# Optimization experiments

Hardware: AMD Instinct MI355X
Metric: run time of the kernel (lower is better)

The kernel has to match this reference:

```python
import jax, jax.numpy as jnp
import numpy as np

D, H, O, E, K = 1024, 4096, 1024, 12, 4
N = 8192


def setup_inputs() -> dict:
    key = jax.random.key(0)
    ks = jax.random.split(key, 7)
    s = 0.02
    return {
        "x": jax.random.normal(ks[0], (N, D), dtype=jnp.float32),
        "gate_w": jax.random.normal(ks[1], (D, E), dtype=jnp.float32) * s,
        "gate_b": jnp.zeros((E,), dtype=jnp.float32),
        "w1": jax.random.normal(ks[2], (E, D, H), dtype=jnp.float32) * s,
        "b1": jnp.zeros((E, H), dtype=jnp.float32),
        "w2": jax.random.normal(ks[3], (E, H, O), dtype=jnp.float32) * s,
        "b2": jnp.zeros((E, O), dtype=jnp.float32),
    }


def reference(x, gate_w, gate_b, w1, b1, w2, b2):
    # Gating: full softmax over all experts, then mask to top-k and renormalize
    scores = x @ gate_w + gate_b                      # [N, E]
    _, topk_idx = jax.lax.top_k(scores, K)            # [N, K]
    mask = jnp.sum(jax.nn.one_hot(topk_idx, E, dtype=scores.dtype), axis=-2)  # [N, E]
    weights = jax.nn.softmax(scores, axis=-1) * mask
    weights = weights / (jnp.sum(weights, axis=-1, keepdims=True) + 1e-8)

    # Dense all-expert MLP (faithful to original: every expert on every token)
    h = jax.nn.relu(jnp.einsum("nd,edh->neh", x, w1) + b1)  # [N, E, H]
    outs = jnp.einsum("neh,eho->neo", h, w2) + b2           # [N, E, O]

    return jnp.einsum("ne,neo->no", weights, outs)          # [N, O]
```

## Files before the change

kernel.cpp:

```cpp
#include <hip/hip_runtime.h>
#include <stdint.h>

#define D_DIM 1024
#define H_DIM 4096
#define O_DIM 1024
#define E_NUM 12
#define TOPK 4
#define N_TOK 8192

#define PAIR_CAP 34304

typedef __bf16 bf16x8 __attribute__((ext_vector_type(8)));
typedef float f32x4 __attribute__((ext_vector_type(4)));
typedef unsigned short u16x8 __attribute__((ext_vector_type(8)));

typedef __attribute__((address_space(3))) unsigned int lds_uint;
typedef __attribute__((address_space(1))) const unsigned int glob_uint;

static __device__ __forceinline__ unsigned short f2b(float f) {
  union { float f; unsigned u; } v; v.f = f;
  unsigned r = v.u + 0x7FFFu + ((v.u >> 16) & 1u);
  return (unsigned short)(r >> 16);
}

static __device__ __forceinline__ void gload16(const void* g, void* l) {
  __builtin_amdgcn_global_load_lds((glob_uint*)g, (lds_uint*)l, 16, 0, 0);
}

__global__ __launch_bounds__(256) void cvt_x_kernel(const float* __restrict__ x,
                                                    unsigned short* __restrict__ xb) {
  int i = blockIdx.x * 256 + threadIdx.x;
  const float4* p = reinterpret_cast<const float4*>(x);
  float4 a = p[2 * i], b = p[2 * i + 1];
  uint4 st;
  st.x = (unsigned)f2b(a.x) | ((unsigned)f2b(a.y) << 16);
  st.y = (unsigned)f2b(a.z) | ((unsigned)f2b(a.w) << 16);
  st.z = (unsigned)f2b(b.x) | ((unsigned)f2b(b.y) << 16);
  st.w = (unsigned)f2b(b.z) | ((unsigned)f2b(b.w) << 16);
  reinterpret_cast<uint4*>(xb)[i] = st;
}

__global__ __launch_bounds__(256) void transpose_cvt_kernel(const float* __restrict__ in,
                                                            unsigned short* __restrict__ out,
                                                            int R, int C) {
  __shared__ float tile[32][33];
  int e = blockIdx.z;
  size_t base = (size_t)e * R * C;
  int c0 = blockIdx.x * 32, r0 = blockIdx.y * 32;
  int tx = threadIdx.x, ty = threadIdx.y;
#pragma unroll
  for (int i = 0; i < 32; i += 8)
    tile[ty + i][tx] = in[base + (size_t)(r0 + ty + i) * C + (c0 + tx)];
  __syncthreads();
#pragma unroll
  for (int i = 0; i < 32; i += 8)
    out[base + (size_t)(c0 + ty + i) * R + (r0 + tx)] = f2b(tile[tx][ty + i]);
}

__global__ __launch_bounds__(256) void gwt_kernel(const float* __restrict__ gw,
                                                  float* __restrict__ gwT) {
  int e = blockIdx.x;
#pragma unroll
  for (int i = 0; i < 4; i++) {
    int d = i * 256 + threadIdx.x;
    gwT[e * D_DIM + d] = gw[(size_t)d * E_NUM + e];
  }
}

__global__ __launch_bounds__(256) void gating_kernel(const float* __restrict__ x,
                                                     const float* __restrict__ gwT,
                                                     const float* __restrict__ gb,
                                                     int* __restrict__ tk_e,
                                                     float* __restrict__ tk_w) {
  int wv = (blockIdx.x * 256 + threadIdx.x) >> 6;
  int lane = threadIdx.x & 63;
  int n0 = wv * 4;
  if (n0 >= N_TOK) return;

  const float4* x4 = reinterpret_cast<const float4*>(x);
  const float4* g4 = reinterpret_cast<const float4*>(gwT);

  float acc[4][E_NUM];
#pragma unroll
  for (int t = 0; t < 4; t++)
#pragma unroll
    for (int e = 0; e < E_NUM; e++) acc[t][e] = 0.f;

#pragma unroll
  for (int i = 0; i < 4; i++) {
    float4 xv[4];
#pragma unroll
    for (int t = 0; t < 4; t++) xv[t] = x4[(size_t)(n0 + t) * 256 + i * 64 + lane];
#pragma unroll
    for (int e = 0; e < E_NUM; e++) {
      float4 g = g4[e * 256 + i * 64 + lane];
#pragma unroll
      for (int t = 0; t < 4; t++) {
        acc[t][e] += xv[t].x * g.x + xv[t].y * g.y + xv[t].z * g.z + xv[t].w * g.w;
      }
    }
  }

#pragma unroll
  for (int t = 0; t < 4; t++)
#pragma unroll
    for (int e = 0; e < E_NUM; e++) {
      float v = acc[t][e];
#pragma unroll
      for (int s = 32; s > 0; s >>= 1) v += __shfl_xor(v, s, 64);
      acc[t][e] = v;
    }

#pragma unroll
  for (int t = 0; t < 4; t++) {
    if (lane == t) {
      int n = n0 + t;
      float sc[E_NUM], sm[E_NUM];
      float mx = -1e30f;
#pragma unroll
      for (int e = 0; e < E_NUM; e++) { sc[e] = acc[t][e] + gb[e]; mx = fmaxf(mx, sc[e]); }
      float Z = 0.f;
#pragma unroll
      for (int e = 0; e < E_NUM; e++) { sm[e] = expf(sc[e] - mx); Z += sm[e]; }
      bool used[E_NUM];
#pragma unroll
      for (int e = 0; e < E_NUM; e++) used[e] = false;
      int eid[TOPK]; float p[TOPK]; float wsum = 0.f;
      for (int k = 0; k < TOPK; k++) {
        float best = -1e30f; int bi = 0;
        for (int e = 0; e < E_NUM; e++)
          if (!used[e] && sc[e] > best) { best = sc[e]; bi = e; }
        used[bi] = true; eid[k] = bi; p[k] = sm[bi] / Z; wsum += p[k];
      }
      float inv = 1.f / (wsum + 1e-8f);
      for (int k = 0; k < TOPK; k++) {
        tk_e[n * TOPK + k] = eid[k];
        tk_w[n * TOPK + k] = p[k] * inv;
      }
    }
  }
}

__global__ __launch_bounds__(256) void hist_rank_kernel(const int* __restrict__ tk_e,
                                                        int* __restrict__ lr,
                                                        int* __restrict__ bc) {
  int blk = blockIdx.x, t = threadIdx.x;
  int n = blk * 256 + t;
  int4 te = reinterpret_cast<const int4*>(tk_e)[n];
  int lane = t & 63, w = t >> 6;
  __shared__ int wt[4][E_NUM];
  int r0 = 0, r1 = 0, r2 = 0, r3 = 0;
#pragma unroll
  for (int e = 0; e < E_NUM; e++) {
    int flag = (te.x == e) || (te.y == e) || (te.z == e) || (te.w == e);
    unsigned long long m = __ballot(flag);
    int rw = __popcll(m & ((1ull << lane) - 1ull));
    if (lane == 0) wt[w][e] = __popcll(m);
    if (te.x == e) r0 = rw;
    if (te.y == e) r1 = rw;
    if (te.z == e) r2 = rw;
    if (te.w == e) r3 = rw;
  }
  __syncthreads();
#pragma unroll
  for (int e = 0; e < E_NUM; e++) {
    int base = 0;
#pragma unroll
    for (int w2 = 0; w2 < 4; w2++)
      if (w2 < w) base += wt[w2][e];
    if (te.x == e) r0 += base;
    if (te.y == e) r1 += base;
    if (te.z == e) r2 += base;
    if (te.w == e) r3 += base;
  }
  int4 out; out.x = r0; out.y = r1; out.z = r2; out.w = r3;
  reinterpret_cast<int4*>(lr)[n] = out;
  if (t == 0) {
#pragma unroll
    for (int e = 0; e < E_NUM; e++)
      bc[blk * E_NUM + e] = wt[0][e] + wt[1][e] + wt[2][e] + wt[3][e];
  }
}

__global__ __launch_bounds__(64) void scan2_kernel(const int* __restrict__ bc,
                                                   int* __restrict__ poff,
                                                   int* __restrict__ bb) {
  int t = threadIdx.x;
  __shared__ int cnte[E_NUM];
  __shared__ int spoff[E_NUM + 1];
  if (t < E_NUM) {
    int s = 0;
#pragma unroll
    for (int b = 0; b < 32; b++) s += bc[b * E_NUM + t];
    cnte[t] = s;
  }
  __syncthreads();
  if (t == 0) {
    int off = 0; spoff[0] = 0;
    for (int e = 0; e < E_NUM; e++) {
      off += ((cnte[e] + 127) >> 7) << 7;
      spoff[e + 1] = off;
    }
  }
  __syncthreads();
  if (t < E_NUM + 1) poff[t] = spoff[t];
  if (t < E_NUM) {
    int run = spoff[t];
    for (int b = 0; b < 32; b++) {
      bb[b * E_NUM + t] = run;
      run += bc[b * E_NUM + t];
    }
  }
}

__global__ __launch_bounds__(256) void fill_pairs_kernel(int* __restrict__ pt) {
  int i = blockIdx.x * 256 + threadIdx.x;
  if (i < PAIR_CAP) pt[i] = 0;
}

__global__ __launch_bounds__(256) void scatter2_kernel(const int* __restrict__ tk_e,
                                                       int* __restrict__ lr_ip,
                                                       const int* __restrict__ bb,
                                                       int* __restrict__ pt) {
  int n = blockIdx.x * 256 + threadIdx.x;
  if (n >= N_TOK) return;
  int blk = n >> 8;
  int4 te = reinterpret_cast<const int4*>(tk_e)[n];
  int4 l4 = reinterpret_cast<const int4*>(lr_ip)[n];
  int p0 = bb[blk * E_NUM + te.x] + l4.x;
  int p1 = bb[blk * E_NUM + te.y] + l4.y;
  int p2 = bb[blk * E_NUM + te.z] + l4.z;
  int p3 = bb[blk * E_NUM + te.w] + l4.w;
  pt[p0] = n; pt[p1] = n; pt[p2] = n; pt[p3] = n;
  int4 ip; ip.x = p0; ip.y = p1; ip.z = p2; ip.w = p3;
  reinterpret_cast<int4*>(lr_ip)[n] = ip;
}


__global__ __launch_bounds__(256, 2) void gemm1_kernel(
    const unsigned short* __restrict__ xb,
    const unsigned short* __restrict__ w1t,
    const float* __restrict__ b1,
    const int* __restrict__ pair_token,
    const int* __restrict__ poff,
    unsigned short* __restrict__ hbuf,
    int tile0) {
  __shared__ unsigned short As[128 * 32];
  __shared__ unsigned short Bs[128 * 32];
  int t = tile0 + blockIdx.y;
  int totTiles = poff[E_NUM] >> 7;
  if (t >= totTiles) return;
  int rowg0 = t << 7;
  int e = 0;
#pragma unroll
  for (int i = 1; i < E_NUM; i++) e += (rowg0 >= poff[i]);

  const int tid = threadIdx.x;
  const int lane = tid & 63, wave = tid >> 6;
  const int wm = wave >> 1, wn = wave & 1;
  const int fr = lane & 15, fgq = lane >> 4;

  const int srow = tid >> 2;
  const int skc = (((tid & 3) ^ ((srow >> 1) & 3)) << 3);
  int tok0 = pair_token[rowg0 + srow];
  int tok1 = pair_token[rowg0 + 64 + srow];
  const unsigned short* a0 = xb + (size_t)tok0 * D_DIM + skc;
  const unsigned short* a1 = xb + (size_t)tok1 * D_DIM + skc;
  int n0 = blockIdx.x << 7;
  const unsigned short* wb = w1t + (size_t)e * H_DIM * D_DIM;
  const unsigned short* b0p = wb + (size_t)(n0 + srow) * D_DIM + skc;
  const unsigned short* b1p = wb + (size_t)(n0 + 64 + srow) * D_DIM + skc;
  unsigned short* lA0 = &As[tid * 8];
  unsigned short* lA1 = &As[2048 + tid * 8];
  unsigned short* lB0 = &Bs[tid * 8];
  unsigned short* lB1 = &Bs[2048 + tid * 8];

  const int cswz = (fgq ^ ((fr >> 1) & 3)) << 3;
  int aoff[4], boff[4];
#pragma unroll
  for (int mf = 0; mf < 4; mf++) aoff[mf] = (wm * 64 + mf * 16 + fr) * 32 + cswz;
#pragma unroll
  for (int nf = 0; nf < 4; nf++) boff[nf] = (wn * 64 + nf * 16 + fr) * 32 + cswz;

  f32x4 acc[4][4];
#pragma unroll
  for (int i = 0; i < 4; i++)
#pragma unroll
    for (int j = 0; j < 4; j++) acc[i][j] = (f32x4){0.f, 0.f, 0.f, 0.f};

  for (int kt = 0; kt < D_DIM / 32; ++kt) {
    int k0 = kt * 32;
    gload16(a0 + k0, lA0);
    gload16(a1 + k0, lA1);
    gload16(b0p + k0, lB0);
    gload16(b1p + k0, lB1);
    __syncthreads();
    bf16x8 af[4], bq[4];
#pragma unroll
    for (int mf = 0; mf < 4; mf++)
      af[mf] = *reinterpret_cast<const bf16x8*>(&As[aoff[mf]]);
#pragma unroll
    for (int nf = 0; nf < 4; nf++)
      bq[nf] = *reinterpret_cast<const bf16x8*>(&Bs[boff[nf]]);
#pragma unroll
    for (int mf = 0; mf < 4; mf++)
#pragma unroll
      for (int nf = 0; nf < 4; nf++)
        acc[mf][nf] = __builtin_amdgcn_mfma_f32_16x16x32_bf16(af[mf], bq[nf], acc[mf][nf], 0, 0, 0);
    __syncthreads();
  }

  int lrow0 = blockIdx.y << 7;
#pragma unroll
  for (int nf = 0; nf < 4; nf++) {
    int col = n0 + wn * 64 + nf * 16 + fr;
    float bias = b1[e * H_DIM + col];
#pragma unroll
    for (int mf = 0; mf < 4; mf++) {
      int m = wm * 64 + mf * 16 + fgq * 4;
#pragma unroll
      for (int r = 0; r < 4; r++) {
        float v = fmaxf(acc[mf][nf][r] + bias, 0.f);
        hbuf[(size_t)(lrow0 + m + r) * H_DIM + col] = f2b(v);
      }
    }
  }
}

__global__ __launch_bounds__(256, 2) void gemm2_kernel(
    const unsigned short* __restrict__ hbuf,
    const unsigned short* __restrict__ w2t,
    const float* __restrict__ b2,
    const int* __restrict__ poff,
    unsigned short* __restrict__ youts,
    int tile0, int nsplit) {
  __shared__ unsigned short As[128 * 32];
  __shared__ unsigned short Bs[128 * 32];
  int t = tile0 + blockIdx.y;
  int totTiles = poff[E_NUM] >> 7;
  if (t >= totTiles) return;
  int rowg0 = t << 7;
  int e = 0;
#pragma unroll
  for (int i = 1; i < E_NUM; i++) e += (rowg0 >= poff[i]);

  const int tid = threadIdx.x;
  const int lane = tid & 63, wave = tid >> 6;
  const int wm = wave >> 1, wn = wave & 1;
  const int fr = lane & 15, fgq = lane >> 4;
  const int z = blockIdx.z;
  const int kspan = H_DIM / nsplit;
  const int kbase = z * kspan;

  const int srow = tid >> 2;
  const int skc = (((tid & 3) ^ ((srow >> 1) & 3)) << 3);
  int lrowb = blockIdx.y << 7;
  const unsigned short* a0 = hbuf + (size_t)(lrowb + srow) * H_DIM + kbase + skc;
  const unsigned short* a1 = hbuf + (size_t)(lrowb + 64 + srow) * H_DIM + kbase + skc;
  int n0 = blockIdx.x << 7;
  const unsigned short* wb = w2t + (size_t)e * O_DIM * H_DIM;
  const unsigned short* b0p = wb + (size_t)(n0 + srow) * H_DIM + kbase + skc;
  const unsigned short* b1p = wb + (size_t)(n0 + 64 + srow) * H_DIM + kbase + skc;
  unsigned short* lA0 = &As[tid * 8];
  unsigned short* lA1 = &As[2048 + tid * 8];
  unsigned short* lB0 = &Bs[tid * 8];
  unsigned short* lB1 = &Bs[2048 + tid * 8];

  const int cswz = (fgq ^ ((fr >> 1) & 3)) << 3;
  int aoff[4], boff[4];
#pragma unroll
  for (int mf = 0; mf < 4; mf++) aoff[mf] = (wm * 64 + mf * 16 + fr) * 32 + cswz;
#pragma unroll
  for (int nf = 0; nf < 4; nf++) boff[nf] = (wn * 64 + nf * 16 + fr) * 32 + cswz;

  f32x4 acc[4][4];
#pragma unroll
  for (int i = 0; i < 4; i++)
#pragma unroll
    for (int j = 0; j < 4; j++) acc[i][j] = (f32x4){0.f, 0.f, 0.f, 0.f};

  for (int kt = 0; kt < kspan / 32; ++kt) {
    int k0 = kt * 32;
    gload16(a0 + k0, lA0);
    gload16(a1 + k0, lA1);
    gload16(b0p + k0, lB0);
    gload16(b1p + k0, lB1);
    __syncthreads();
    bf16x8 af[4], bq[4];
#pragma unroll
    for (int mf = 0; mf < 4; mf++)
      af[mf] = *reinterpret_cast<const bf16x8*>(&As[aoff[mf]]);
#pragma unroll
    for (int nf = 0; nf < 4; nf++)
      bq[nf] = *reinterpret_cast<const bf16x8*>(&Bs[boff[nf]]);
#pragma unroll
    for (int mf = 0; mf < 4; mf++)
#pragma unroll
      for (int nf = 0; nf < 4; nf++)
        acc[mf][nf] = __builtin_amdgcn_mfma_f32_16x16x32_bf16(af[mf], bq[nf], acc[mf][nf], 0, 0, 0);
    __syncthreads();
  }

  size_t ybase = (size_t)z * PAIR_CAP;
#pragma unroll
  for (int nf = 0; nf < 4; nf++) {
    int col = n0 + wn * 64 + nf * 16 + fr;
    float bias = (z == 0) ? b2[e * O_DIM + col] : 0.f;
#pragma unroll
    for (int mf = 0; mf < 4; mf++) {
      int m = wm * 64 + mf * 16 + fgq * 4;
#pragma unroll
      for (int r = 0; r < 4; r++) {
        float v = acc[mf][nf][r] + bias;
        youts[(ybase + rowg0 + m + r) * O_DIM + col] = f2b(v);
      }
    }
  }
}

static __device__ __forceinline__ void acc8(float* a, const unsigned short* y, float wk) {
  u16x8 v = *reinterpret_cast<const u16x8*>(y);
#pragma unroll
  for (int j = 0; j < 8; j++)
    a[j] += wk * __uint_as_float((unsigned)v[j] << 16);
}

__global__ __launch_bounds__(256) void reduce_kernel(const unsigned short* __restrict__ youts,
                                                     const int* __restrict__ ip,
                                                     const float* __restrict__ tk_w,
                                                     float* __restrict__ out,
                                                     int nsplit) {
  int gid = blockIdx.x * 256 + threadIdx.x;
  int n = gid >> 7;
  int c0 = (gid & 127) << 3;
  int4 p = reinterpret_cast<const int4*>(ip)[n];
  float4 w = reinterpret_cast<const float4*>(tk_w)[n];
  const size_t zoff = (size_t)PAIR_CAP * O_DIM;
  float a[8];
#pragma unroll
  for (int j = 0; j < 8; j++) a[j] = 0.f;
  {
    const unsigned short* y = youts + (size_t)p.x * O_DIM + c0;
    acc8(a, y, w.x);
    if (nsplit == 2) acc8(a, y + zoff, w.x);
  }
  {
    const unsigned short* y = youts + (size_t)p.y * O_DIM + c0;
    acc8(a, y, w.y);
    if (nsplit == 2) acc8(a, y + zoff, w.y);
  }
  {
    const unsigned short* y = youts + (size_t)p.z * O_DIM + c0;
    acc8(a, y, w.z);
    if (nsplit == 2) acc8(a, y + zoff, w.z);
  }
  {
    const unsigned short* y = youts + (size_t)p.w * O_DIM + c0;
    acc8(a, y, w.w);
    if (nsplit == 2) acc8(a, y + zoff, w.w);
  }
  float* orow = out + (size_t)n * O_DIM + c0;
  float4 o0; o0.x = a[0]; o0.y = a[1]; o0.z = a[2]; o0.w = a[3];
  float4 o1; o1.x = a[4]; o1.y = a[5]; o1.z = a[6]; o1.w = a[7];
  reinterpret_cast<float4*>(orow)[0] = o0;
  reinterpret_cast<float4*>(orow)[1] = o1;
}

extern "C" void kernel_launch(void* const* d_in, const int* in_sizes, int n_in,
                              void* d_out, int out_size, void* d_ws, size_t ws_size,
                              hipStream_t stream) {
  const float* x  = (const float*)d_in[0];
  const float* gw = (const float*)d_in[1];
  const float* gb = (const float*)d_in[2];
  const float* w1 = (const float*)d_in[3];
  const float* b1 = (const float*)d_in[4];
  const float* w2 = (const float*)d_in[5];
  const float* b2 = (const float*)d_in[6];
  float* out = (float*)d_out;

  char* ws = (char*)d_ws;
  size_t off = 0;
  auto alloc = [&](size_t bytes) -> void* {
    void* p = ws + off;
    off = (off + bytes + 255) & ~(size_t)255;
    return p;
  };
  unsigned short* xb   = (unsigned short*)alloc((size_t)N_TOK * D_DIM * 2);
  unsigned short* w1t  = (unsigned short*)alloc((size_t)E_NUM * H_DIM * D_DIM * 2);
  unsigned short* w2t  = (unsigned short*)alloc((size_t)E_NUM * O_DIM * H_DIM * 2);
  float* gwT  = (float*)alloc((size_t)E_NUM * D_DIM * 4);
  int*   tk_e = (int*)alloc((size_t)N_TOK * TOPK * 4);
  float* tk_w = (float*)alloc((size_t)N_TOK * TOPK * 4);
  int*   lr   = (int*)alloc((size_t)N_TOK * TOPK * 4);
  int*   pt   = (int*)alloc((size_t)PAIR_CAP * 4);
  int*   bc   = (int*)alloc(32 * E_NUM * 4);
  int*   bb   = (int*)alloc(32 * E_NUM * 4);
  int*   poff = (int*)alloc(64);

  const size_t HB134 = (size_t)134 * 128 * H_DIM * 2;
  const size_t HB67  = (size_t)67 * 128 * H_DIM * 2;
  const size_t YO    = (size_t)PAIR_CAP * O_DIM * 2;
  int TPC, NCH, NS;
  if (ws_size >= off + HB134 + 2 * YO + 1024)      { TPC = 134; NCH = 2; NS = 2; }
  else if (ws_size >= off + HB134 + YO + 1024)     { TPC = 134; NCH = 2; NS = 1; }
  else                                             { TPC = 67;  NCH = 4; NS = 1; }
  unsigned short* hbuf  = (unsigned short*)alloc((size_t)TPC * 128 * H_DIM * 2);
  unsigned short* youts = (unsigned short*)alloc((size_t)NS * YO);
  if (off > ws_size) return;

  cvt_x_kernel<<<N_TOK * D_DIM / 8 / 256, 256, 0, stream>>>(x, xb);
  transpose_cvt_kernel<<<dim3(H_DIM / 32, D_DIM / 32, E_NUM), dim3(32, 8), 0, stream>>>(w1, w1t, D_DIM, H_DIM);
  transpose_cvt_kernel<<<dim3(O_DIM / 32, H_DIM / 32, E_NUM), dim3(32, 8), 0, stream>>>(w2, w2t, H_DIM, O_DIM);
  gwt_kernel<<<E_NUM, 256, 0, stream>>>(gw, gwT);
  gating_kernel<<<N_TOK / 16, 256, 0, stream>>>(x, gwT, gb, tk_e, tk_w);
  hist_rank_kernel<<<N_TOK / 256, 256, 0, stream>>>(tk_e, lr, bc);
  scan2_kernel<<<1, 64, 0, stream>>>(bc, poff, bb);
  fill_pairs_kernel<<<(PAIR_CAP + 255) / 256, 256, 0, stream>>>(pt);
  scatter2_kernel<<<N_TOK / 256, 256, 0, stream>>>(tk_e, lr, bb, pt);

  for (int c = 0; c < NCH; c++) {
    int tile0 = c * TPC;
    gemm1_kernel<<<dim3(H_DIM / 128, TPC), 256, 0, stream>>>(xb, w1t, b1, pt, poff, hbuf, tile0);
    gemm2_kernel<<<dim3(O_DIM / 128, TPC, NS), 256, 0, stream>>>(hbuf, w2t, b2, poff, youts, tile0, NS);
  }
  reduce_kernel<<<N_TOK * (O_DIM / 8) / 256, 256, 0, stream>>>(youts, lr, tk_w, out, NS);
}
```

Before: 1.002 ms.

## Remap GEMM blocks to a 1D XCD-aware order and drop split-K when memory allows

Both expert GEMM kernels now launch on a flat 1D grid. The block index is remapped so that consecutive blocks on the same XCD (blockIdx.x & 7) take contiguous tiles, with the row tile as the fastest-varying index, so blocks sharing a weight column block land on the same chiplet's L2. The workspace selection also changes: with enough memory it now uses a single K split (NS=1) instead of NS=2, and NS=2 is used only in a fallback config with smaller chunks. This aims to improve L2 reuse of weights across MI355X XCDs and to cut the split-K youts traffic. In exchange, gemm2 gets less grid parallelism and an extra integer div/mod per block.

```diff
diff --git a/kernel.cpp b/kernel.cpp
--- a/kernel.cpp
+++ b/kernel.cpp
@@ -244,10 +244,15 @@
     const int* __restrict__ pair_token,
     const int* __restrict__ poff,
     unsigned short* __restrict__ hbuf,
-    int tile0) {
+    int tile0, int tpc) {
   __shared__ unsigned short As[128 * 32];
   __shared__ unsigned short Bs[128 * 32];
-  int t = tile0 + blockIdx.y;
+  int cpx = gridDim.x >> 3;
+  int f = (blockIdx.x & 7) * cpx + (blockIdx.x >> 3);
+  int tile = f % tpc;
+  int colb = f / tpc;
+
+  int t = tile0 + tile;
   int totTiles = poff[E_NUM] >> 7;
   if (t >= totTiles) return;
   int rowg0 = t << 7;
@@ -266,7 +271,7 @@
   int tok1 = pair_token[rowg0 + 64 + srow];
   const unsigned short* a0 = xb + (size_t)tok0 * D_DIM + skc;
   const unsigned short* a1 = xb + (size_t)tok1 * D_DIM + skc;
-  int n0 = blockIdx.x << 7;
+  int n0 = colb << 7;
   const unsigned short* wb = w1t + (size_t)e * H_DIM * D_DIM;
   const unsigned short* b0p = wb + (size_t)(n0 + srow) * D_DIM + skc;
   const unsigned short* b1p = wb + (size_t)(n0 + 64 + srow) * D_DIM + skc;
@@ -310,7 +315,7 @@
     __syncthreads();
   }
 
-  int lrow0 = blockIdx.y << 7;
+  int lrow0 = tile << 7;
 #pragma unroll
   for (int nf = 0; nf < 4; nf++) {
     int col = n0 + wn * 64 + nf * 16 + fr;
@@ -333,10 +338,17 @@
     const float* __restrict__ b2,
     const int* __restrict__ poff,
     unsigned short* __restrict__ youts,
-    int tile0, int nsplit) {
+    int tile0, int tpc, int nsplit) {
   __shared__ unsigned short As[128 * 32];
   __shared__ unsigned short Bs[128 * 32];
-  int t = tile0 + blockIdx.y;
+  int cpx = gridDim.x >> 3;
+  int f = (blockIdx.x & 7) * cpx + (blockIdx.x >> 3);
+  int tile = f % tpc;
+  int rest = f / tpc;
+  int z = rest % nsplit;
+  int colb = rest / nsplit;
+
+  int t = tile0 + tile;
   int totTiles = poff[E_NUM] >> 7;
   if (t >= totTiles) return;
   int rowg0 = t << 7;
@@ -348,16 +360,15 @@
   const int lane = tid & 63, wave = tid >> 6;
   const int wm = wave >> 1, wn = wave & 1;
   const int fr = lane & 15, fgq = lane >> 4;
-  const int z = blockIdx.z;
   const int kspan = H_DIM / nsplit;
   const int kbase = z * kspan;
 
   const int srow = tid >> 2;
   const int skc = (((tid & 3) ^ ((srow >> 1) & 3)) << 3);
-  int lrowb = blockIdx.y << 7;
+  int lrowb = tile << 7;
   const unsigned short* a0 = hbuf + (size_t)(lrowb + srow) * H_DIM + kbase + skc;
   const unsigned short* a1 = hbuf + (size_t)(lrowb + 64 + srow) * H_DIM + kbase + skc;
-  int n0 = blockIdx.x << 7;
+  int n0 = colb << 7;
   const unsigned short* wb = w2t + (size_t)e * O_DIM * H_DIM;
   const unsigned short* b0p = wb + (size_t)(n0 + srow) * H_DIM + kbase + skc;
   const unsigned short* b1p = wb + (size_t)(n0 + 64 + srow) * H_DIM + kbase + skc;
@@ -501,8 +512,8 @@
   const size_t HB67  = (size_t)67 * 128 * H_DIM * 2;
   const size_t YO    = (size_t)PAIR_CAP * O_DIM * 2;
   int TPC, NCH, NS;
-  if (ws_size >= off + HB134 + 2 * YO + 1024)      { TPC = 134; NCH = 2; NS = 2; }
-  else if (ws_size >= off + HB134 + YO + 1024)     { TPC = 134; NCH = 2; NS = 1; }
+  if (ws_size >= off + HB134 + YO + 1024)          { TPC = 134; NCH = 2; NS = 1; }
+  else if (ws_size >= off + HB67 + 2 * YO + 1024)  { TPC = 67;  NCH = 4; NS = 2; }
   else                                             { TPC = 67;  NCH = 4; NS = 1; }
   unsigned short* hbuf  = (unsigned short*)alloc((size_t)TPC * 128 * H_DIM * 2);
   unsigned short* youts = (unsigned short*)alloc((size_t)NS * YO);
@@ -520,8 +531,8 @@
 
   for (int c = 0; c < NCH; c++) {
     int tile0 = c * TPC;
-    gemm1_kernel<<<dim3(H_DIM / 128, TPC), 256, 0, stream>>>(xb, w1t, b1, pt, poff, hbuf, tile0);
-    gemm2_kernel<<<dim3(O_DIM / 128, TPC, NS), 256, 0, stream>>>(hbuf, w2t, b2, poff, youts, tile0, NS);
+    gemm1_kernel<<<dim3((H_DIM / 128) * TPC), 256, 0, stream>>>(xb, w1t, b1, pt, poff, hbuf, tile0, TPC);
+    gemm2_kernel<<<dim3((O_DIM / 128) * TPC * NS), 256, 0, stream>>>(hbuf, w2t, b2, poff, youts, tile0, TPC, NS);
   }
   reduce_kernel<<<N_TOK * (O_DIM / 8) / 256, 256, 0, stream>>>(youts, lr, tk_w, out, NS);
 }
```

Result: slower. 1.120 ms (+11.8%).
